# Kernel tuning notes

Measured on AMD Instinct MI355X. Metric: run time of the kernel, lower is better.

The kernel has to match this reference:

```python
import jax, jax.numpy as jnp
import numpy as np

N_LAYERS = 3
H = 128
N_NODES = 10000
N_EDGES = 160000
EPS = 1e-5

def silu(x):
    return x * jax.nn.sigmoid(x)

def batchnorm(x, gamma, beta):
    # BatchNorm1d, training-mode statistics (biased variance), over the node/edge dim
    mu = x.mean(axis=0)
    var = x.var(axis=0)
    return gamma * (x - mu) * jax.lax.rsqrt(var + EPS) + beta

def _forward(edge_index, emb_nodes, emb_edges, pre_Wn, pre_bn, pre_We, pre_be,
             We1, be1, We2, be2, Wx1, bx1, Wx2, bx2, Wh1, bh1, Wh2, bh2,
             gam_n, bet_n, gam_e, bet_e):
    src, dst = edge_index[0], edge_index[1]
    N = emb_nodes.shape[0]
    coords = emb_nodes                      # [N, 3] equivariant coordinates
    V = emb_nodes @ pre_Wn + pre_bn         # [N, H]
    E = emb_edges @ pre_We + pre_be         # [Ne, H] (overwritten by mij each layer)
    for l in range(N_LAYERS):
        diff = coords[dst] - coords[src]                          # [Ne, 3]
        dist = jnp.sqrt(jnp.sum(diff * diff, axis=-1, keepdims=True))  # [Ne, 1]
        h = jnp.concatenate([V[src], V[dst], dist, emb_edges], axis=-1)  # [Ne, 2H+3]
        mij = silu(silu(h @ We1[l] + be1[l]) @ We2[l] + be2[l])   # phi_e -> [Ne, H]
        px = silu(mij @ Wx1[l] + bx1[l]) @ Wx2[l] + bx2[l]        # phi_x -> [Ne, 3]
        # equivariant coordinate update; graph_node_index is None -> M = N
        coords = coords + jax.ops.segment_sum(diff * px, dst, num_segments=N) / (N - 1)
        mi = jax.ops.segment_sum(mij, dst, num_segments=N)        # [N, H]
        V = silu(jnp.concatenate([V, mi], axis=-1) @ Wh1[l] + bh1[l]) @ Wh2[l] + bh2[l]
        E = mij
        # encoder: act -> BatchNorm -> Dropout(eval = identity)
        V = batchnorm(jax.nn.elu(V), gam_n[l], bet_n[l])
        E = batchnorm(jax.nn.elu(E), gam_e[l], bet_e[l])
    return V, E

def setup_inputs() -> dict:
    key = jax.random.key(0)
    ks = iter(jax.random.split(key, 32))
    def rn(shape, scale=0.05):
        return jax.random.normal(next(ks), shape, dtype=jnp.float32) * scale
    src = jax.random.randint(next(ks), (N_EDGES,), 0, N_NODES)
    off = jax.random.randint(next(ks), (N_EDGES,), 1, N_NODES)
    dst = (src + off) % N_NODES  # no self-loops -> distance never exactly 0
    edge_index = jnp.stack([src, dst]).astype(jnp.int64) if jax.config.jax_enable_x64 else jnp.stack([src, dst])
    return dict(
        emb_nodes=jax.random.normal(next(ks), (N_NODES, 3), dtype=jnp.float32),
        emb_edges=jax.random.normal(next(ks), (N_EDGES, 2), dtype=jnp.float32),
        edge_index=edge_index,
        pre_Wn=rn((3, H)), pre_bn=jnp.zeros((H,), jnp.float32),
        pre_We=rn((2, H)), pre_be=jnp.zeros((H,), jnp.float32),
        We1=rn((N_LAYERS, 2 * H + 3, H)), be1=jnp.zeros((N_LAYERS, H), jnp.float32),
        We2=rn((N_LAYERS, H, H)), be2=jnp.zeros((N_LAYERS, H), jnp.float32),
        Wx1=rn((N_LAYERS, H, H)), bx1=jnp.zeros((N_LAYERS, H), jnp.float32),
        Wx2=rn((N_LAYERS, H, 3)), bx2=jnp.zeros((N_LAYERS, 3), jnp.float32),
        Wh1=rn((N_LAYERS, 2 * H, H)), bh1=jnp.zeros((N_LAYERS, H), jnp.float32),
        Wh2=rn((N_LAYERS, H, H)), bh2=jnp.zeros((N_LAYERS, H), jnp.float32),
        gam_n=jnp.ones((N_LAYERS, H), jnp.float32), bet_n=jnp.zeros((N_LAYERS, H), jnp.float32),
        gam_e=jnp.ones((N_LAYERS, H), jnp.float32), bet_e=jnp.zeros((N_LAYERS, H), jnp.float32),
    )

def reference(emb_nodes, emb_edges, edge_index, pre_Wn, pre_bn, pre_We, pre_be,
              We1, be1, We2, be2, Wx1, bx1, Wx2, bx2, Wh1, bh1, Wh2, bh2,
              gam_n, bet_n, gam_e, bet_e):
    return _forward(edge_index, emb_nodes, emb_edges, pre_Wn, pre_bn, pre_We, pre_be,
                    We1, be1, We2, be2, Wx1, bx1, Wx2, bx2, Wh1, bh1, Wh2, bh2,
                    gam_n, bet_n, gam_e, bet_e)
```

## Files before the change

kernel.cpp:

```cpp
#include <hip/hip_runtime.h>
#include <hip/hip_bf16.h>
#include <math.h>

#define NN 10000
#define NE 160000
#define HH 128
#define EPSBN 1e-5f

typedef __attribute__((ext_vector_type(8))) short s8b;
typedef __attribute__((ext_vector_type(4))) float f32x4;

#define MFMA16 __builtin_amdgcn_mfma_f32_16x16x32_bf16

__device__ __forceinline__ float silu_f(float x) { return x / (1.f + __expf(-x)); }
__device__ __forceinline__ float elu_f(float x)  { return x > 0.f ? x : expm1f(x); }

__device__ __forceinline__ ushort rnb(float x) {
    unsigned u = __float_as_uint(x);
    unsigned r = (u + 0x7fffu + ((u >> 16) & 1u)) >> 16;
    return (ushort)r;
}
__device__ __forceinline__ float bf2f(ushort u) {
    return __uint_as_float(((unsigned)u) << 16);
}
__device__ __forceinline__ s8b ldg8(const ushort* p) { return *(const s8b*)p; }

__global__ void k_zero(float* __restrict__ p, int n) {
    int i = blockIdx.x * blockDim.x + threadIdx.x;
    if (i < n) p[i] = 0.f;
}
__global__ void k_zero_int(int* __restrict__ p, int n) {
    int i = blockIdx.x * blockDim.x + threadIdx.x;
    if (i < n) p[i] = 0;
}
__global__ void k_copy(const float* __restrict__ a, float* __restrict__ b, int n) {
    int i = blockIdx.x * blockDim.x + threadIdx.x;
    if (i < n) b[i] = a[i];
}

__global__ void k_vinit(const float* __restrict__ en, const float* __restrict__ Wn,
                        const float* __restrict__ bn, ushort* __restrict__ Vb) {
    int idx = blockIdx.x * blockDim.x + threadIdx.x;
    if (idx >= NN * HH) return;
    int i = idx >> 7, j = idx & 127;
    float v = fmaf(en[i * 3 + 0], Wn[j], bn[j]);
    v = fmaf(en[i * 3 + 1], Wn[HH + j], v);
    v = fmaf(en[i * 3 + 2], Wn[2 * HH + j], v);
    Vb[idx] = rnb(v);
}

__global__ void k_wprep(const float* __restrict__ We1, const float* __restrict__ We2,
                        const float* __restrict__ Wx1, const float* __restrict__ Wh1,
                        const float* __restrict__ Wh2, ushort* __restrict__ Wb) {
    int idx = blockIdx.x * 256 + threadIdx.x;
    if (idx >= 344064) return;
    int layer = idx / 114688;
    int r = idx - layer * 114688;
    const float* src; int K; int roff;
    if (r < 32768)      { src = We1 + (size_t)layer * 33152; K = 256; roff = r; }
    else if (r < 49152) { src = We2 + (size_t)layer * 16384; K = 128; roff = r - 32768; }
    else if (r < 65536) { src = Wx1 + (size_t)layer * 16384; K = 128; roff = r - 49152; }
    else if (r < 98304) { src = Wh1 + (size_t)layer * 32768; K = 256; roff = r - 65536; }
    else                { src = Wh2 + (size_t)layer * 16384; K = 128; roff = r - 98304; }
    int n = roff / K, k = roff - n * K;
    Wb[idx] = rnb(src[k * 128 + n]);
}

__global__ void k_wx2prep(const float* __restrict__ Wx2, ushort* __restrict__ Wx2b) {
    int idx = blockIdx.x * 256 + threadIdx.x;
    if (idx >= 3 * 16 * 128) return;
    int layer = idx / 2048;
    int r = idx - layer * 2048;
    int n = r >> 7, k = r & 127;
    Wx2b[idx] = (n < 3) ? rnb(Wx2[layer * 384 + k * 3 + n]) : (ushort)0;
}

__global__ void k_hist(const int* __restrict__ dst, int* __restrict__ deg) {
    int e = blockIdx.x * blockDim.x + threadIdx.x;
    if (e < NE) atomicAdd(&deg[dst[e]], 1);
}
__global__ __launch_bounds__(256)
void k_scan(const int* __restrict__ deg, int* __restrict__ offs, int* __restrict__ cur) {
    __shared__ int part[256];
    const int t = threadIdx.x;
    const int s0 = t * 40, s1 = min(s0 + 40, NN);
    int s = 0;
    for (int i = s0; i < s1; ++i) s += deg[i];
    part[t] = s;
    __syncthreads();
    if (t == 0) {
        int r = 0;
        for (int i = 0; i < 256; ++i) { int v = part[i]; part[i] = r; r += v; }
    }
    __syncthreads();
    int r = part[t];
    for (int i = s0; i < s1; ++i) { offs[i] = r; cur[i] = r; r += deg[i]; }
    if (t == 255) offs[NN] = r;
}
__global__ void k_fill(const int* __restrict__ dst, int* __restrict__ cur, int* __restrict__ eid) {
    int e = blockIdx.x * blockDim.x + threadIdx.x;
    if (e < NE) {
        int p = atomicAdd(&cur[dst[e]], 1);
        eid[p] = e;
    }
}

__global__ __launch_bounds__(512, 2)
void k_efused(const ushort* __restrict__ Vb,
              const int* __restrict__ src, const int* __restrict__ dst,
              const float* __restrict__ coords, const float* __restrict__ ee,
              const ushort* __restrict__ W1b,
              const float* __restrict__ We1f, const float* __restrict__ be1,
              const ushort* __restrict__ W2b,
              const float* __restrict__ be2,
              const ushort* __restrict__ Wxb,
              const float* __restrict__ bx1,
              const ushort* __restrict__ Wx2b,
              const float* __restrict__ bx2,
              ushort* __restrict__ mijb, float4* __restrict__ cd4) {
    __shared__ ushort t1b[4][128][40];
    __shared__ int sid[128], did[128];
    __shared__ float dd[128], eAa[128], eBb[128];
    __shared__ float d3[3][128];
    const int t = threadIdx.x;
    const int lane = t & 63;
    const int w = t >> 6;
    const int wr = w >> 1, wc = w & 1;
    const int e0 = blockIdx.x * 128;
    if (t < 128) {
        int e = e0 + t;
        int s = src[e], d = dst[e];
        sid[t] = s; did[t] = d;
        float dx = coords[d * 3 + 0] - coords[s * 3 + 0];
        float dy = coords[d * 3 + 1] - coords[s * 3 + 1];
        float dz = coords[d * 3 + 2] - coords[s * 3 + 2];
        dd[t] = sqrtf(dx * dx + dy * dy + dz * dz);
        d3[0][t] = dx; d3[1][t] = dy; d3[2][t] = dz;
        eAa[t] = ee[2 * e]; eBb[t] = ee[2 * e + 1];
    }
    __syncthreads();
    const int l15 = lane & 15, lq = lane >> 4;
    f32x4 acc[2][4];
#pragma unroll
    for (int i = 0; i < 2; ++i)
#pragma unroll
        for (int j = 0; j < 4; ++j) acc[i][j] = (f32x4){0.f, 0.f, 0.f, 0.f};

#pragma unroll
    for (int half = 0; half < 2; ++half) {
        const int* ids = half ? did : sid;
#pragma unroll
        for (int kt = 0; kt < 4; ++kt) {
            const int wk = half * 128 + kt * 32;
            s8b a[2], b[4];
#pragma unroll
            for (int mi = 0; mi < 2; ++mi) {
                int row = ids[wr * 32 + mi * 16 + l15];
                a[mi] = ldg8(Vb + (size_t)row * HH + kt * 32 + lq * 8);
            }
#pragma unroll
            for (int ni = 0; ni < 4; ++ni) {
                int col = wc * 64 + ni * 16 + l15;
                b[ni] = ldg8(W1b + (size_t)col * 256 + wk + lq * 8);
            }
#pragma unroll
            for (int mi = 0; mi < 2; ++mi)
#pragma unroll
                for (int ni = 0; ni < 4; ++ni)
                    acc[mi][ni] = MFMA16(a[mi], b[ni], acc[mi][ni], 0, 0, 0);
        }
    }
#pragma unroll
    for (int mi = 0; mi < 2; ++mi)
#pragma unroll
        for (int ni = 0; ni < 4; ++ni) {
            int col = wc * 64 + ni * 16 + l15;
            float w256 = We1f[256 * HH + col];
            float w257 = We1f[257 * HH + col];
            float w258 = We1f[258 * HH + col];
            float bi = be1[col];
            int kt = col >> 5, c = col & 31;
#pragma unroll
            for (int r = 0; r < 4; ++r) {
                int m = wr * 32 + mi * 16 + lq * 4 + r;
                float v = acc[mi][ni][r] + bi;
                v = fmaf(dd[m], w256, v);
                v = fmaf(eAa[m], w257, v);
                v = fmaf(eBb[m], w258, v);
                t1b[kt][m][c] = rnb(silu_f(v));
                acc[mi][ni][r] = 0.f;
            }
        }
    __syncthreads();
#pragma unroll
    for (int kt = 0; kt < 4; ++kt) {
        s8b a[2], b[4];
#pragma unroll
        for (int mi = 0; mi < 2; ++mi) {
            int row = wr * 32 + mi * 16 + l15;
            a[mi] = *(const s8b*)&t1b[kt][row][lq * 8];
        }
#pragma unroll
        for (int ni = 0; ni < 4; ++ni) {
            int col = wc * 64 + ni * 16 + l15;
            b[ni] = ldg8(W2b + (size_t)col * 128 + kt * 32 + lq * 8);
        }
#pragma unroll
        for (int mi = 0; mi < 2; ++mi)
#pragma unroll
            for (int ni = 0; ni < 4; ++ni)
                acc[mi][ni] = MFMA16(a[mi], b[ni], acc[mi][ni], 0, 0, 0);
    }
    __syncthreads();
#pragma unroll
    for (int mi = 0; mi < 2; ++mi)
#pragma unroll
        for (int ni = 0; ni < 4; ++ni) {
            int col = wc * 64 + ni * 16 + l15;
            float bi = be2[col];
            int kt = col >> 5, c = col & 31;
#pragma unroll
            for (int r = 0; r < 4; ++r) {
                int m = wr * 32 + mi * 16 + lq * 4 + r;
                ushort mv = rnb(silu_f(acc[mi][ni][r] + bi));
                mijb[(size_t)(e0 + m) * HH + col] = mv;
                t1b[kt][m][c] = mv;
                acc[mi][ni][r] = 0.f;
            }
        }
    __syncthreads();
#pragma unroll
    for (int kt = 0; kt < 4; ++kt) {
        s8b a[2], b[4];
#pragma unroll
        for (int mi = 0; mi < 2; ++mi) {
            int row = wr * 32 + mi * 16 + l15;
            a[mi] = *(const s8b*)&t1b[kt][row][lq * 8];
        }
#pragma unroll
        for (int ni = 0; ni < 4; ++ni) {
            int col = wc * 64 + ni * 16 + l15;
            b[ni] = ldg8(Wxb + (size_t)col * 128 + kt * 32 + lq * 8);
        }
#pragma unroll
        for (int mi = 0; mi < 2; ++mi)
#pragma unroll
            for (int ni = 0; ni < 4; ++ni)
                acc[mi][ni] = MFMA16(a[mi], b[ni], acc[mi][ni], 0, 0, 0);
    }
    __syncthreads();
#pragma unroll
    for (int mi = 0; mi < 2; ++mi)
#pragma unroll
        for (int ni = 0; ni < 4; ++ni) {
            int col = wc * 64 + ni * 16 + l15;
            float bi = bx1[col];
            int kt = col >> 5, c = col & 31;
#pragma unroll
            for (int r = 0; r < 4; ++r) {
                int m = wr * 32 + mi * 16 + lq * 4 + r;
                t1b[kt][m][c] = rnb(silu_f(acc[mi][ni][r] + bi));
            }
        }
    __syncthreads();
    f32x4 accd = (f32x4){0.f, 0.f, 0.f, 0.f};
#pragma unroll
    for (int kt = 0; kt < 4; ++kt) {
        s8b a = *(const s8b*)&t1b[kt][w * 16 + l15][lq * 8];
        s8b b = ldg8(Wx2b + (size_t)l15 * 128 + kt * 32 + lq * 8);
        accd = MFMA16(a, b, accd, 0, 0, 0);
    }
    if (l15 < 3) {
        float bi = bx2[l15];
#pragma unroll
        for (int r = 0; r < 4; ++r) {
            int row = w * 16 + lq * 4 + r;
            float px = accd[r] + bi;
            ((float*)&cd4[e0 + row])[l15] = d3[l15][row] * px;
        }
    }
}

__global__ __launch_bounds__(128)
void k_mi(const ushort* __restrict__ mijb, const int* __restrict__ offs,
          const int* __restrict__ eid, ushort* __restrict__ mib) {
    const int n = blockIdx.x;
    const int t = threadIdx.x;
    const int b = offs[n], e = offs[n + 1];
    float s = 0.f;
    for (int j = b; j < e; ++j)
        s += bf2f(mijb[(size_t)eid[j] * HH + t]);
    mib[(size_t)n * HH + t] = rnb(s);
}

__global__ void k_coordupd(float* __restrict__ coords, const float4* __restrict__ cd4,
                           const int* __restrict__ offs, const int* __restrict__ eid) {
    int idx = blockIdx.x * blockDim.x + threadIdx.x;
    if (idx >= NN * 3) return;
    int n = idx / 3, c = idx - 3 * n;
    int b = offs[n], e = offs[n + 1];
    float s = 0.f;
    for (int j = b; j < e; ++j)
        s += ((const float*)&cd4[eid[j]])[c];
    coords[idx] += s * (1.f / (NN - 1));
}

__global__ __launch_bounds__(256, 4)
void k_nfused(const ushort* __restrict__ Vb, const ushort* __restrict__ mib,
              const ushort* __restrict__ Whb,
              const float* __restrict__ bh1,
              const ushort* __restrict__ Wgb,
              const float* __restrict__ bh2,
              float* __restrict__ X,
              float* __restrict__ ssum, float* __restrict__ ssq) {
    __shared__ ushort tb[4][64][40];
    const int t = threadIdx.x;
    const int lane = t & 63;
    const int w = t >> 6;
    const int wr = w >> 1, wc = w & 1;
    const int r0 = blockIdx.x * 64;
    const int l15 = lane & 15, lq = lane >> 4;
    f32x4 acc[2][4];
#pragma unroll
    for (int i = 0; i < 2; ++i)
#pragma unroll
        for (int j = 0; j < 4; ++j) acc[i][j] = (f32x4){0.f, 0.f, 0.f, 0.f};

#pragma unroll
    for (int kk = 0; kk < 8; ++kk) {
        const ushort* Ap = (kk < 4) ? Vb : mib;
        const int k0 = (kk & 3) * 32;
        s8b a[2], b[4];
#pragma unroll
        for (int mi_ = 0; mi_ < 2; ++mi_) {
            int row = r0 + wr * 32 + mi_ * 16 + l15;
            if (row >= NN) row = NN - 1;
            a[mi_] = ldg8(Ap + (size_t)row * HH + k0 + lq * 8);
        }
#pragma unroll
        for (int ni = 0; ni < 4; ++ni) {
            int col = wc * 64 + ni * 16 + l15;
            b[ni] = ldg8(Whb + (size_t)col * 256 + kk * 32 + lq * 8);
        }
#pragma unroll
        for (int mi_ = 0; mi_ < 2; ++mi_)
#pragma unroll
            for (int ni = 0; ni < 4; ++ni)
                acc[mi_][ni] = MFMA16(a[mi_], b[ni], acc[mi_][ni], 0, 0, 0);
    }
#pragma unroll
    for (int mi_ = 0; mi_ < 2; ++mi_)
#pragma unroll
        for (int ni = 0; ni < 4; ++ni) {
            int col = wc * 64 + ni * 16 + l15;
            float bi = bh1[col];
            int kt = col >> 5, c = col & 31;
#pragma unroll
            for (int r = 0; r < 4; ++r) {
                int m = wr * 32 + mi_ * 16 + lq * 4 + r;
                tb[kt][m][c] = rnb(silu_f(acc[mi_][ni][r] + bi));
                acc[mi_][ni][r] = 0.f;
            }
        }
    __syncthreads();
#pragma unroll
    for (int kt = 0; kt < 4; ++kt) {
        s8b a[2], b[4];
#pragma unroll
        for (int mi_ = 0; mi_ < 2; ++mi_) {
            int row = wr * 32 + mi_ * 16 + l15;
            a[mi_] = *(const s8b*)&tb[kt][row][lq * 8];
        }
#pragma unroll
        for (int ni = 0; ni < 4; ++ni) {
            int col = wc * 64 + ni * 16 + l15;
            b[ni] = ldg8(Wgb + (size_t)col * 128 + kt * 32 + lq * 8);
        }
#pragma unroll
        for (int mi_ = 0; mi_ < 2; ++mi_)
#pragma unroll
            for (int ni = 0; ni < 4; ++ni)
                acc[mi_][ni] = MFMA16(a[mi_], b[ni], acc[mi_][ni], 0, 0, 0);
    }
    float s[4] = {0.f, 0.f, 0.f, 0.f}, q[4] = {0.f, 0.f, 0.f, 0.f};
#pragma unroll
    for (int mi_ = 0; mi_ < 2; ++mi_)
#pragma unroll
        for (int ni = 0; ni < 4; ++ni) {
            int col = wc * 64 + ni * 16 + l15;
            float bi = bh2[col];
#pragma unroll
            for (int r = 0; r < 4; ++r) {
                int m = r0 + wr * 32 + mi_ * 16 + lq * 4 + r;
                float v = elu_f(acc[mi_][ni][r] + bi);
                if (m < NN) {
                    X[(size_t)m * HH + col] = v;
                    s[ni] += v; q[ni] += v * v;
                }
            }
        }
#pragma unroll
    for (int j = 0; j < 4; ++j) {
        s[j] += __shfl_xor(s[j], 16);
        s[j] += __shfl_xor(s[j], 32);
        q[j] += __shfl_xor(q[j], 16);
        q[j] += __shfl_xor(q[j], 32);
    }
    if (lane < 16) {
#pragma unroll
        for (int j = 0; j < 4; ++j) {
            int col = wc * 64 + j * 16 + l15;
            atomicAdd(&ssum[col], s[j]);
            atomicAdd(&ssq[col], q[j]);
        }
    }
}

__global__ void k_bnorm_nodes(const float* __restrict__ X, const float* __restrict__ ssum,
                              const float* __restrict__ ssq, const float* __restrict__ gam,
                              const float* __restrict__ bet, float* __restrict__ outf,
                              ushort* __restrict__ outb, int writeb) {
    int idx = blockIdx.x * blockDim.x + threadIdx.x;
    if (idx >= NN * HH) return;
    int c = idx & 127;
    float mu = ssum[c] * (1.f / NN);
    float var = ssq[c] * (1.f / NN) - mu * mu;
    float v = fmaf(gam[c] * (X[idx] - mu), rsqrtf(var + EPSBN), bet[c]);
    if (writeb) outb[idx] = rnb(v);
    else        outf[idx] = v;
}

__global__ __launch_bounds__(256)
void k_estats(const ushort* __restrict__ mijb, float* __restrict__ ssum, float* __restrict__ ssq) {
    const int t = threadIdx.x;
    const int col = t & 127;
    const int half = t >> 7;
    const int rbase = blockIdx.x * 250;
    float s = 0.f, q = 0.f;
    for (int r = rbase + half; r < rbase + 250; r += 2) {
        float x = elu_f(bf2f(mijb[(size_t)r * HH + col]));
        s += x; q += x * x;
    }
    atomicAdd(&ssum[col], s);
    atomicAdd(&ssq[col], q);
}

__global__ void k_bnorm_edges(const ushort* __restrict__ mijb, const float* __restrict__ ssum,
                              const float* __restrict__ ssq, const float* __restrict__ gam,
                              const float* __restrict__ bet, float* __restrict__ out) {
    size_t stride = (size_t)gridDim.x * blockDim.x;
    for (size_t idx = (size_t)blockIdx.x * blockDim.x + threadIdx.x; idx < (size_t)NE * HH; idx += stride) {
        int c = (int)(idx & 127);
        float x = elu_f(bf2f(mijb[idx]));
        float mu = ssum[c] * (1.f / NE);
        float var = ssq[c] * (1.f / NE) - mu * mu;
        out[idx] = fmaf(gam[c] * (x - mu), rsqrtf(var + EPSBN), bet[c]);
    }
}

extern "C" void kernel_launch(void* const* d_in, const int* in_sizes, int n_in,
                              void* d_out, int out_size, void* d_ws, size_t ws_size,
                              hipStream_t stream) {
    (void)in_sizes; (void)n_in; (void)out_size; (void)ws_size;
    const float* emb_nodes = (const float*)d_in[0];
    const float* emb_edges = (const float*)d_in[1];
    const int*   eidx      = (const int*)d_in[2];
    const float* pre_Wn = (const float*)d_in[3];
    const float* pre_bn = (const float*)d_in[4];
    const float* We1 = (const float*)d_in[7];
    const float* be1 = (const float*)d_in[8];
    const float* We2 = (const float*)d_in[9];
    const float* be2 = (const float*)d_in[10];
    const float* Wx1 = (const float*)d_in[11];
    const float* bx1 = (const float*)d_in[12];
    const float* Wx2 = (const float*)d_in[13];
    const float* bx2 = (const float*)d_in[14];
    const float* Wh1 = (const float*)d_in[15];
    const float* bh1 = (const float*)d_in[16];
    const float* Wh2 = (const float*)d_in[17];
    const float* bh2 = (const float*)d_in[18];
    const float* gam_n = (const float*)d_in[19];
    const float* bet_n = (const float*)d_in[20];
    const float* gam_e = (const float*)d_in[21];
    const float* bet_e = (const float*)d_in[22];

    const int* src = eidx;
    const int* dst = eidx + NE;

    float* ws = (float*)d_ws;
    float*   coords = ws;
    ushort*  Vb     = (ushort*)(ws + 30000);
    ushort*  mib    = (ushort*)(ws + 670000);
    float*   X      = ws + 1310000;
    float4*  cd4    = (float4*)(ws + 2590000);
    ushort*  mijb   = (ushort*)(ws + 3230000);
    float*   snN    = ws + 13470000;
    float*   sqN    = ws + 13470128;
    float*   snE    = ws + 13470256;
    float*   sqE    = ws + 13470384;
    ushort*  Wb     = (ushort*)(ws + 13470512);
    ushort*  Wx2b   = (ushort*)(ws + 13642544);
    int*     I0     = (int*)(ws + 13645616);
    int*     deg    = I0;
    int*     offs   = I0 + 10000;
    int*     cur    = I0 + 20001;
    int*     eid    = I0 + 30001;

    float* outV = (float*)d_out;
    float* outE = (float*)d_out + (size_t)NN * HH;

    k_copy<<<(30000 + 255) / 256, 256, 0, stream>>>(emb_nodes, coords, 30000);
    k_vinit<<<(NN * HH + 255) / 256, 256, 0, stream>>>(emb_nodes, pre_Wn, pre_bn, Vb);
    k_wprep<<<1344, 256, 0, stream>>>(We1, We2, Wx1, Wh1, Wh2, Wb);
    k_wx2prep<<<24, 256, 0, stream>>>(Wx2, Wx2b);

    k_zero_int<<<(NN + 255) / 256, 256, 0, stream>>>(deg, NN);
    k_hist<<<(NE + 255) / 256, 256, 0, stream>>>(dst, deg);
    k_scan<<<1, 256, 0, stream>>>(deg, offs, cur);
    k_fill<<<(NE + 255) / 256, 256, 0, stream>>>(dst, cur, eid);

    for (int l = 0; l < 3; ++l) {
        const float* We1l = We1 + (size_t)l * 259 * 128;
        const float* be1l = be1 + l * 128;
        const float* be2l = be2 + l * 128;
        const float* bx1l = bx1 + l * 128;
        const float* bx2l = bx2 + l * 3;
        const float* bh1l = bh1 + l * 128;
        const float* bh2l = bh2 + l * 128;
        const size_t L = (size_t)l * 114688;
        const ushort* W1b = Wb + L;
        const ushort* W2b = Wb + L + 32768;
        const ushort* Wxb = Wb + L + 49152;
        const ushort* Whb = Wb + L + 65536;
        const ushort* Wgb = Wb + L + 98304;
        const ushort* Wx2bl = Wx2b + (size_t)l * 2048;

        k_zero<<<2, 256, 0, stream>>>(snN, 512);
        k_efused<<<NE / 128, 512, 0, stream>>>(Vb, src, dst, coords, emb_edges,
                                               W1b, We1l, be1l, W2b, be2l,
                                               Wxb, bx1l, Wx2bl, bx2l, mijb, cd4);
        k_mi<<<NN, 128, 0, stream>>>(mijb, offs, eid, mib);
        k_coordupd<<<(NN * 3 + 255) / 256, 256, 0, stream>>>(coords, cd4, offs, eid);
        k_nfused<<<(NN + 63) / 64, 256, 0, stream>>>(Vb, mib, Whb, bh1l, Wgb, bh2l, X, snN, sqN);
        k_bnorm_nodes<<<(NN * HH + 255) / 256, 256, 0, stream>>>(X, snN, sqN, gam_n + l * 128,
                                                                 bet_n + l * 128,
                                                                 outV, Vb, (l < 2) ? 1 : 0);
        if (l == 2) {
            k_estats<<<640, 256, 0, stream>>>(mijb, snE, sqE);
            k_bnorm_edges<<<4096, 256, 0, stream>>>(mijb, snE, sqE, gam_e + l * 128, bet_e + l * 128, outE);
        }
    }
}
```

Baseline: 843.6 us.

## Software-pipeline MFMA operand loads and shrink node-MLP tile to 32 rows

In the edge MLP kernel, the gathered V rows and weight fragments are now double-buffered in registers, so the next k-step's global loads are in flight while the current MFMAs run. The src/dst indices go straight into registers instead of through shared memory, and the per-column We1 tail weights are hoisted ahead of the first barrier. The node MLP kernel switches to 32-row tiles with one M fragment per wave, launching twice as many blocks to raise parallelism. BN stat zeroing becomes a single launch over per-layer buffers, and bf16 rounding uses the library conversion, at the cost of extra registers for the prefetch buffers.

```diff
diff --git a/kernel.cpp b/kernel.cpp
--- a/kernel.cpp
+++ b/kernel.cpp
@@ -15,15 +15,14 @@
 __device__ __forceinline__ float silu_f(float x) { return x / (1.f + __expf(-x)); }
 __device__ __forceinline__ float elu_f(float x)  { return x > 0.f ? x : expm1f(x); }
 
-__device__ __forceinline__ ushort rnb(float x) {
-    unsigned u = __float_as_uint(x);
-    unsigned r = (u + 0x7fffu + ((u >> 16) & 1u)) >> 16;
-    return (ushort)r;
+__device__ __forceinline__ ushort f2b(float x) {
+    __hip_bfloat16 h = __float2bfloat16(x);
+    return *reinterpret_cast<ushort*>(&h);
 }
 __device__ __forceinline__ float bf2f(ushort u) {
     return __uint_as_float(((unsigned)u) << 16);
 }
-__device__ __forceinline__ s8b ldg8(const ushort* p) { return *(const s8b*)p; }
+__device__ __forceinline__ s8b ldg8(const ushort* p) { return *(const s8b*)(p); }
 
 __global__ void k_zero(float* __restrict__ p, int n) {
     int i = blockIdx.x * blockDim.x + threadIdx.x;
@@ -46,7 +45,7 @@
     float v = fmaf(en[i * 3 + 0], Wn[j], bn[j]);
     v = fmaf(en[i * 3 + 1], Wn[HH + j], v);
     v = fmaf(en[i * 3 + 2], Wn[2 * HH + j], v);
-    Vb[idx] = rnb(v);
+    Vb[idx] = f2b(v);
 }
 
 __global__ void k_wprep(const float* __restrict__ We1, const float* __restrict__ We2,
@@ -63,7 +62,7 @@
     else if (r < 98304) { src = Wh1 + (size_t)layer * 32768; K = 256; roff = r - 65536; }
     else                { src = Wh2 + (size_t)layer * 16384; K = 128; roff = r - 98304; }
     int n = roff / K, k = roff - n * K;
-    Wb[idx] = rnb(src[k * 128 + n]);
+    Wb[idx] = f2b(src[k * 128 + n]);
 }
 
 __global__ void k_wx2prep(const float* __restrict__ Wx2, ushort* __restrict__ Wx2b) {
@@ -72,7 +71,7 @@
     int layer = idx / 2048;
     int r = idx - layer * 2048;
     int n = r >> 7, k = r & 127;
-    Wx2b[idx] = (n < 3) ? rnb(Wx2[layer * 384 + k * 3 + n]) : (ushort)0;
+    Wx2b[idx] = (n < 3) ? f2b(Wx2[layer * 384 + k * 3 + n]) : (ushort)0;
 }
 
 __global__ void k_hist(const int* __restrict__ dst, int* __restrict__ deg) {
@@ -119,7 +118,6 @@
               const float* __restrict__ bx2,
               ushort* __restrict__ mijb, float4* __restrict__ cd4) {
     __shared__ ushort t1b[4][128][40];
-    __shared__ int sid[128], did[128];
     __shared__ float dd[128], eAa[128], eBb[128];
     __shared__ float d3[3][128];
     const int t = threadIdx.x;
@@ -127,10 +125,26 @@
     const int w = t >> 6;
     const int wr = w >> 1, wc = w & 1;
     const int e0 = blockIdx.x * 128;
+    const int l15 = lane & 15, lq = lane >> 4;
+
+    const int er0 = e0 + wr * 32 + l15;
+    const int er1 = er0 + 16;
+    const int rS0 = src[er0], rS1 = src[er1];
+    const int rD0 = dst[er0], rD1 = dst[er1];
+
+    float w256[4], w257[4], w258[4], bi1[4];
+#pragma unroll
+    for (int ni = 0; ni < 4; ++ni) {
+        int col = wc * 64 + ni * 16 + l15;
+        w256[ni] = We1f[256 * HH + col];
+        w257[ni] = We1f[257 * HH + col];
+        w258[ni] = We1f[258 * HH + col];
+        bi1[ni]  = be1[col];
+    }
+
     if (t < 128) {
         int e = e0 + t;
         int s = src[e], d = dst[e];
-        sid[t] = s; did[t] = d;
         float dx = coords[d * 3 + 0] - coords[s * 3 + 0];
         float dy = coords[d * 3 + 1] - coords[s * 3 + 1];
         float dz = coords[d * 3 + 2] - coords[s * 3 + 2];
@@ -138,78 +152,89 @@
         d3[0][t] = dx; d3[1][t] = dy; d3[2][t] = dz;
         eAa[t] = ee[2 * e]; eBb[t] = ee[2 * e + 1];
     }
-    __syncthreads();
-    const int l15 = lane & 15, lq = lane >> 4;
+
     f32x4 acc[2][4];
 #pragma unroll
     for (int i = 0; i < 2; ++i)
 #pragma unroll
         for (int j = 0; j < 4; ++j) acc[i][j] = (f32x4){0.f, 0.f, 0.f, 0.f};
 
-#pragma unroll
-    for (int half = 0; half < 2; ++half) {
-        const int* ids = half ? did : sid;
-#pragma unroll
-        for (int kt = 0; kt < 4; ++kt) {
-            const int wk = half * 128 + kt * 32;
-            s8b a[2], b[4];
-#pragma unroll
-            for (int mi = 0; mi < 2; ++mi) {
-                int row = ids[wr * 32 + mi * 16 + l15];
-                a[mi] = ldg8(Vb + (size_t)row * HH + kt * 32 + lq * 8);
-            }
-#pragma unroll
-            for (int ni = 0; ni < 4; ++ni) {
-                int col = wc * 64 + ni * 16 + l15;
-                b[ni] = ldg8(W1b + (size_t)col * 256 + wk + lq * 8);
-            }
-#pragma unroll
-            for (int mi = 0; mi < 2; ++mi)
-#pragma unroll
-                for (int ni = 0; ni < 4; ++ni)
-                    acc[mi][ni] = MFMA16(a[mi], b[ni], acc[mi][ni], 0, 0, 0);
-        }
-    }
+    const ushort* wb1 = W1b + (size_t)(wc * 64 + l15) * 256 + lq * 8;
+    s8b a0 = ldg8(Vb + (size_t)rS0 * HH + lq * 8);
+    s8b a1 = ldg8(Vb + (size_t)rS1 * HH + lq * 8);
+    s8b b0 = ldg8(wb1);
+    s8b b1 = ldg8(wb1 + 16 * 256);
+    s8b b2 = ldg8(wb1 + 32 * 256);
+    s8b b3 = ldg8(wb1 + 48 * 256);
+#pragma unroll
+    for (int s = 0; s < 8; ++s) {
+        s8b na0, na1, nb0, nb1, nb2, nb3;
+        if (s < 7) {
+            const int sn = s + 1;
+            const int kt = sn & 3;
+            const int r0 = (sn < 4) ? rS0 : rD0;
+            const int r1 = (sn < 4) ? rS1 : rD1;
+            na0 = ldg8(Vb + (size_t)r0 * HH + kt * 32 + lq * 8);
+            na1 = ldg8(Vb + (size_t)r1 * HH + kt * 32 + lq * 8);
+            nb0 = ldg8(wb1 + sn * 32);
+            nb1 = ldg8(wb1 + 16 * 256 + sn * 32);
+            nb2 = ldg8(wb1 + 32 * 256 + sn * 32);
+            nb3 = ldg8(wb1 + 48 * 256 + sn * 32);
+        }
+        acc[0][0] = MFMA16(a0, b0, acc[0][0], 0, 0, 0);
+        acc[0][1] = MFMA16(a0, b1, acc[0][1], 0, 0, 0);
+        acc[0][2] = MFMA16(a0, b2, acc[0][2], 0, 0, 0);
+        acc[0][3] = MFMA16(a0, b3, acc[0][3], 0, 0, 0);
+        acc[1][0] = MFMA16(a1, b0, acc[1][0], 0, 0, 0);
+        acc[1][1] = MFMA16(a1, b1, acc[1][1], 0, 0, 0);
+        acc[1][2] = MFMA16(a1, b2, acc[1][2], 0, 0, 0);
+        acc[1][3] = MFMA16(a1, b3, acc[1][3], 0, 0, 0);
+        if (s < 7) { a0 = na0; a1 = na1; b0 = nb0; b1 = nb1; b2 = nb2; b3 = nb3; }
+    }
+    __syncthreads();
 #pragma unroll
     for (int mi = 0; mi < 2; ++mi)
 #pragma unroll
         for (int ni = 0; ni < 4; ++ni) {
             int col = wc * 64 + ni * 16 + l15;
-            float w256 = We1f[256 * HH + col];
-            float w257 = We1f[257 * HH + col];
-            float w258 = We1f[258 * HH + col];
-            float bi = be1[col];
             int kt = col >> 5, c = col & 31;
 #pragma unroll
             for (int r = 0; r < 4; ++r) {
                 int m = wr * 32 + mi * 16 + lq * 4 + r;
-                float v = acc[mi][ni][r] + bi;
-                v = fmaf(dd[m], w256, v);
-                v = fmaf(eAa[m], w257, v);
-                v = fmaf(eBb[m], w258, v);
-                t1b[kt][m][c] = rnb(silu_f(v));
+                float v = acc[mi][ni][r] + bi1[ni];
+                v = fmaf(dd[m], w256[ni], v);
+                v = fmaf(eAa[m], w257[ni], v);
+                v = fmaf(eBb[m], w258[ni], v);
+                t1b[kt][m][c] = f2b(silu_f(v));
                 acc[mi][ni][r] = 0.f;
             }
         }
+    const ushort* wb2 = W2b + (size_t)(wc * 64 + l15) * 128 + lq * 8;
+    b0 = ldg8(wb2);
+    b1 = ldg8(wb2 + 16 * 128);
+    b2 = ldg8(wb2 + 32 * 128);
+    b3 = ldg8(wb2 + 48 * 128);
     __syncthreads();
 #pragma unroll
     for (int kt = 0; kt < 4; ++kt) {
-        s8b a[2], b[4];
-#pragma unroll
-        for (int mi = 0; mi < 2; ++mi) {
-            int row = wr * 32 + mi * 16 + l15;
-            a[mi] = *(const s8b*)&t1b[kt][row][lq * 8];
-        }
-#pragma unroll
-        for (int ni = 0; ni < 4; ++ni) {
-            int col = wc * 64 + ni * 16 + l15;
-            b[ni] = ldg8(W2b + (size_t)col * 128 + kt * 32 + lq * 8);
-        }
-#pragma unroll
-        for (int mi = 0; mi < 2; ++mi)
-#pragma unroll
-            for (int ni = 0; ni < 4; ++ni)
-                acc[mi][ni] = MFMA16(a[mi], b[ni], acc[mi][ni], 0, 0, 0);
+        s8b a0c = *(const s8b*)&t1b[kt][wr * 32 + l15][lq * 8];
+        s8b a1c = *(const s8b*)&t1b[kt][wr * 32 + 16 + l15][lq * 8];
+        s8b nb0, nb1, nb2, nb3;
+        if (kt < 3) {
+            nb0 = ldg8(wb2 + (kt + 1) * 32);
+            nb1 = ldg8(wb2 + 16 * 128 + (kt + 1) * 32);
+            nb2 = ldg8(wb2 + 32 * 128 + (kt + 1) * 32);
+            nb3 = ldg8(wb2 + 48 * 128 + (kt + 1) * 32);
+        }
+        acc[0][0] = MFMA16(a0c, b0, acc[0][0], 0, 0, 0);
+        acc[0][1] = MFMA16(a0c, b1, acc[0][1], 0, 0, 0);
+        acc[0][2] = MFMA16(a0c, b2, acc[0][2], 0, 0, 0);
+        acc[0][3] = MFMA16(a0c, b3, acc[0][3], 0, 0, 0);
+        acc[1][0] = MFMA16(a1c, b0, acc[1][0], 0, 0, 0);
+        acc[1][1] = MFMA16(a1c, b1, acc[1][1], 0, 0, 0);
+        acc[1][2] = MFMA16(a1c, b2, acc[1][2], 0, 0, 0);
+        acc[1][3] = MFMA16(a1c, b3, acc[1][3], 0, 0, 0);
+        if (kt < 3) { b0 = nb0; b1 = nb1; b2 = nb2; b3 = nb3; }
     }
     __syncthreads();
 #pragma unroll
@@ -222,31 +247,38 @@
 #pragma unroll
             for (int r = 0; r < 4; ++r) {
                 int m = wr * 32 + mi * 16 + lq * 4 + r;
-                ushort mv = rnb(silu_f(acc[mi][ni][r] + bi));
+                ushort mv = f2b(silu_f(acc[mi][ni][r] + bi));
                 mijb[(size_t)(e0 + m) * HH + col] = mv;
                 t1b[kt][m][c] = mv;
                 acc[mi][ni][r] = 0.f;
             }
         }
+    const ushort* wbx = Wxb + (size_t)(wc * 64 + l15) * 128 + lq * 8;
+    b0 = ldg8(wbx);
+    b1 = ldg8(wbx + 16 * 128);
+    b2 = ldg8(wbx + 32 * 128);
+    b3 = ldg8(wbx + 48 * 128);
     __syncthreads();
 #pragma unroll
     for (int kt = 0; kt < 4; ++kt) {
-        s8b a[2], b[4];
-#pragma unroll
-        for (int mi = 0; mi < 2; ++mi) {
-            int row = wr * 32 + mi * 16 + l15;
-            a[mi] = *(const s8b*)&t1b[kt][row][lq * 8];
-        }
-#pragma unroll
-        for (int ni = 0; ni < 4; ++ni) {
-            int col = wc * 64 + ni * 16 + l15;
-            b[ni] = ldg8(Wxb + (size_t)col * 128 + kt * 32 + lq * 8);
-        }
-#pragma unroll
-        for (int mi = 0; mi < 2; ++mi)
-#pragma unroll
-            for (int ni = 0; ni < 4; ++ni)
-                acc[mi][ni] = MFMA16(a[mi], b[ni], acc[mi][ni], 0, 0, 0);
+        s8b a0c = *(const s8b*)&t1b[kt][wr * 32 + l15][lq * 8];
+        s8b a1c = *(const s8b*)&t1b[kt][wr * 32 + 16 + l15][lq * 8];
+        s8b nb0, nb1, nb2, nb3;
+        if (kt < 3) {
+            nb0 = ldg8(wbx + (kt + 1) * 32);
+            nb1 = ldg8(wbx + 16 * 128 + (kt + 1) * 32);
+            nb2 = ldg8(wbx + 32 * 128 + (kt + 1) * 32);
+            nb3 = ldg8(wbx + 48 * 128 + (kt + 1) * 32);
+        }
+        acc[0][0] = MFMA16(a0c, b0, acc[0][0], 0, 0, 0);
+        acc[0][1] = MFMA16(a0c, b1, acc[0][1], 0, 0, 0);
+        acc[0][2] = MFMA16(a0c, b2, acc[0][2], 0, 0, 0);
+        acc[0][3] = MFMA16(a0c, b3, acc[0][3], 0, 0, 0);
+        acc[1][0] = MFMA16(a1c, b0, acc[1][0], 0, 0, 0);
+        acc[1][1] = MFMA16(a1c, b1, acc[1][1], 0, 0, 0);
+        acc[1][2] = MFMA16(a1c, b2, acc[1][2], 0, 0, 0);
+        acc[1][3] = MFMA16(a1c, b3, acc[1][3], 0, 0, 0);
+        if (kt < 3) { b0 = nb0; b1 = nb1; b2 = nb2; b3 = nb3; }
     }
     __syncthreads();
 #pragma unroll
@@ -259,7 +291,7 @@
 #pragma unroll
             for (int r = 0; r < 4; ++r) {
                 int m = wr * 32 + mi * 16 + lq * 4 + r;
-                t1b[kt][m][c] = rnb(silu_f(acc[mi][ni][r] + bi));
+                t1b[kt][m][c] = f2b(silu_f(acc[mi][ni][r] + bi));
             }
         }
     __syncthreads();
@@ -290,7 +322,7 @@
     float s = 0.f;
     for (int j = b; j < e; ++j)
         s += bf2f(mijb[(size_t)eid[j] * HH + t]);
-    mib[(size_t)n * HH + t] = rnb(s);
+    mib[(size_t)n * HH + t] = f2b(s);
 }
 
 __global__ void k_coordupd(float* __restrict__ coords, const float4* __restrict__ cd4,
@@ -313,92 +345,93 @@
               const float* __restrict__ bh2,
               float* __restrict__ X,
               float* __restrict__ ssum, float* __restrict__ ssq) {
-    __shared__ ushort tb[4][64][40];
+    __shared__ ushort tb[4][32][40];
     const int t = threadIdx.x;
     const int lane = t & 63;
     const int w = t >> 6;
     const int wr = w >> 1, wc = w & 1;
-    const int r0 = blockIdx.x * 64;
+    const int r0 = blockIdx.x * 32;
     const int l15 = lane & 15, lq = lane >> 4;
-    f32x4 acc[2][4];
-#pragma unroll
-    for (int i = 0; i < 2; ++i)
-#pragma unroll
-        for (int j = 0; j < 4; ++j) acc[i][j] = (f32x4){0.f, 0.f, 0.f, 0.f};
-
-#pragma unroll
-    for (int kk = 0; kk < 8; ++kk) {
-        const ushort* Ap = (kk < 4) ? Vb : mib;
-        const int k0 = (kk & 3) * 32;
-        s8b a[2], b[4];
-#pragma unroll
-        for (int mi_ = 0; mi_ < 2; ++mi_) {
-            int row = r0 + wr * 32 + mi_ * 16 + l15;
-            if (row >= NN) row = NN - 1;
-            a[mi_] = ldg8(Ap + (size_t)row * HH + k0 + lq * 8);
-        }
-#pragma unroll
-        for (int ni = 0; ni < 4; ++ni) {
-            int col = wc * 64 + ni * 16 + l15;
-            b[ni] = ldg8(Whb + (size_t)col * 256 + kk * 32 + lq * 8);
-        }
-#pragma unroll
-        for (int mi_ = 0; mi_ < 2; ++mi_)
-#pragma unroll
-            for (int ni = 0; ni < 4; ++ni)
-                acc[mi_][ni] = MFMA16(a[mi_], b[ni], acc[mi_][ni], 0, 0, 0);
-    }
-#pragma unroll
-    for (int mi_ = 0; mi_ < 2; ++mi_)
-#pragma unroll
-        for (int ni = 0; ni < 4; ++ni) {
-            int col = wc * 64 + ni * 16 + l15;
-            float bi = bh1[col];
-            int kt = col >> 5, c = col & 31;
-#pragma unroll
-            for (int r = 0; r < 4; ++r) {
-                int m = wr * 32 + mi_ * 16 + lq * 4 + r;
-                tb[kt][m][c] = rnb(silu_f(acc[mi_][ni][r] + bi));
-                acc[mi_][ni][r] = 0.f;
+    int rowA = r0 + wr * 16 + l15;
+    if (rowA >= NN) rowA = NN - 1;
+    f32x4 acc[4];
+#pragma unroll
+    for (int j = 0; j < 4; ++j) acc[j] = (f32x4){0.f, 0.f, 0.f, 0.f};
+
+    const ushort* wbh = Whb + (size_t)(wc * 64 + l15) * 256 + lq * 8;
+    s8b a0 = ldg8(Vb + (size_t)rowA * HH + lq * 8);
+    s8b b0 = ldg8(wbh);
+    s8b b1 = ldg8(wbh + 16 * 256);
+    s8b b2 = ldg8(wbh + 32 * 256);
+    s8b b3 = ldg8(wbh + 48 * 256);
+#pragma unroll
+    for (int s = 0; s < 8; ++s) {
+        s8b na0, nb0, nb1, nb2, nb3;
+        if (s < 7) {
+            const int sn = s + 1;
+            const ushort* Ap = (sn < 4) ? Vb : mib;
+            const int k0 = (sn & 3) * 32;
+            na0 = ldg8(Ap + (size_t)rowA * HH + k0 + lq * 8);
+            nb0 = ldg8(wbh + sn * 32);
+            nb1 = ldg8(wbh + 16 * 256 + sn * 32);
+            nb2 = ldg8(wbh + 32 * 256 + sn * 32);
+            nb3 = ldg8(wbh + 48 * 256 + sn * 32);
+        }
+        acc[0] = MFMA16(a0, b0, acc[0], 0, 0, 0);
+        acc[1] = MFMA16(a0, b1, acc[1], 0, 0, 0);
+        acc[2] = MFMA16(a0, b2, acc[2], 0, 0, 0);
+        acc[3] = MFMA16(a0, b3, acc[3], 0, 0, 0);
+        if (s < 7) { a0 = na0; b0 = nb0; b1 = nb1; b2 = nb2; b3 = nb3; }
+    }
+#pragma unroll
+    for (int ni = 0; ni < 4; ++ni) {
+        int col = wc * 64 + ni * 16 + l15;
+        float bi = bh1[col];
+        int kt = col >> 5, c = col & 31;
+#pragma unroll
+        for (int r = 0; r < 4; ++r) {
+            int m = wr * 16 + lq * 4 + r;
+            tb[kt][m][c] = f2b(silu_f(acc[ni][r] + bi));
+            acc[ni][r] = 0.f;
+        }
+    }
+    const ushort* wbg = Wgb + (size_t)(wc * 64 + l15) * 128 + lq * 8;
+    b0 = ldg8(wbg);
+    b1 = ldg8(wbg + 16 * 128);
+    b2 = ldg8(wbg + 32 * 128);
+    b3 = ldg8(wbg + 48 * 128);
+    __syncthreads();
+#pragma unroll
+    for (int kt = 0; kt < 4; ++kt) {
+        s8b a = *(const s8b*)&tb[kt][wr * 16 + l15][lq * 8];
+        s8b nb0, nb1, nb2, nb3;
+        if (kt < 3) {
+            nb0 = ldg8(wbg + (kt + 1) * 32);
+            nb1 = ldg8(wbg + 16 * 128 + (kt + 1) * 32);
+            nb2 = ldg8(wbg + 32 * 128 + (kt + 1) * 32);
+            nb3 = ldg8(wbg + 48 * 128 + (kt + 1) * 32);
+        }
+        acc[0] = MFMA16(a, b0, acc[0], 0, 0, 0);
+        acc[1] = MFMA16(a, b1, acc[1], 0, 0, 0);
+        acc[2] = MFMA16(a, b2, acc[2], 0, 0, 0);
+        acc[3] = MFMA16(a, b3, acc[3], 0, 0, 0);
+        if (kt < 3) { b0 = nb0; b1 = nb1; b2 = nb2; b3 = nb3; }
+    }
+    float s[4] = {0.f, 0.f, 0.f, 0.f}, q[4] = {0.f, 0.f, 0.f, 0.f};
+#pragma unroll
+    for (int ni = 0; ni < 4; ++ni) {
+        int col = wc * 64 + ni * 16 + l15;
+        float bi = bh2[col];
+#pragma unroll
+        for (int r = 0; r < 4; ++r) {
+            int m = r0 + wr * 16 + lq * 4 + r;
+            float v = elu_f(acc[ni][r] + bi);
+            if (m < NN) {
+                X[(size_t)m * HH + col] = v;
+                s[ni] += v; q[ni] += v * v;
             }
         }
-    __syncthreads();
-#pragma unroll
-    for (int kt = 0; kt < 4; ++kt) {
-        s8b a[2], b[4];
-#pragma unroll
-        for (int mi_ = 0; mi_ < 2; ++mi_) {
-            int row = wr * 32 + mi_ * 16 + l15;
-            a[mi_] = *(const s8b*)&tb[kt][row][lq * 8];
-        }
-#pragma unroll
-        for (int ni = 0; ni < 4; ++ni) {
-            int col = wc * 64 + ni * 16 + l15;
-            b[ni] = ldg8(Wgb + (size_t)col * 128 + kt * 32 + lq * 8);
-        }
-#pragma unroll
-        for (int mi_ = 0; mi_ < 2; ++mi_)
-#pragma unroll
-            for (int ni = 0; ni < 4; ++ni)
-                acc[mi_][ni] = MFMA16(a[mi_], b[ni], acc[mi_][ni], 0, 0, 0);
-    }
-    float s[4] = {0.f, 0.f, 0.f, 0.f}, q[4] = {0.f, 0.f, 0.f, 0.f};
-#pragma unroll
-    for (int mi_ = 0; mi_ < 2; ++mi_)
-#pragma unroll
-        for (int ni = 0; ni < 4; ++ni) {
-            int col = wc * 64 + ni * 16 + l15;
-            float bi = bh2[col];
-#pragma unroll
-            for (int r = 0; r < 4; ++r) {
-                int m = r0 + wr * 32 + mi_ * 16 + lq * 4 + r;
-                float v = elu_f(acc[mi_][ni][r] + bi);
-                if (m < NN) {
-                    X[(size_t)m * HH + col] = v;
-                    s[ni] += v; q[ni] += v * v;
-                }
-            }
-        }
+    }
 #pragma unroll
     for (int j = 0; j < 4; ++j) {
         s[j] += __shfl_xor(s[j], 16);
@@ -426,7 +459,7 @@
     float mu = ssum[c] * (1.f / NN);
     float var = ssq[c] * (1.f / NN) - mu * mu;
     float v = fmaf(gam[c] * (X[idx] - mu), rsqrtf(var + EPSBN), bet[c]);
-    if (writeb) outb[idx] = rnb(v);
+    if (writeb) outb[idx] = f2b(v);
     else        outf[idx] = v;
 }
 
@@ -494,13 +527,11 @@
     float*   X      = ws + 1310000;
     float4*  cd4    = (float4*)(ws + 2590000);
     ushort*  mijb   = (ushort*)(ws + 3230000);
-    float*   snN    = ws + 13470000;
-    float*   sqN    = ws + 13470128;
-    float*   snE    = ws + 13470256;
-    float*   sqE    = ws + 13470384;
-    ushort*  Wb     = (ushort*)(ws + 13470512);
-    ushort*  Wx2b   = (ushort*)(ws + 13642544);
-    int*     I0     = (int*)(ws + 13645616);
+    float*   statN  = ws + 13470000;
+    float*   statE  = ws + 13470768;
+    ushort*  Wb     = (ushort*)(ws + 13471024);
+    ushort*  Wx2b   = (ushort*)(ws + 13643056);
+    int*     I0     = (int*)(ws + 13646128);
     int*     deg    = I0;
     int*     offs   = I0 + 10000;
     int*     cur    = I0 + 20001;
@@ -513,6 +544,7 @@
     k_vinit<<<(NN * HH + 255) / 256, 256, 0, stream>>>(emb_nodes, pre_Wn, pre_bn, Vb);
     k_wprep<<<1344, 256, 0, stream>>>(We1, We2, Wx1, Wh1, Wh2, Wb);
     k_wx2prep<<<24, 256, 0, stream>>>(Wx2, Wx2b);
+    k_zero<<<4, 256, 0, stream>>>(statN, 1024);
 
     k_zero_int<<<(NN + 255) / 256, 256, 0, stream>>>(deg, NN);
     k_hist<<<(NE + 255) / 256, 256, 0, stream>>>(dst, deg);
@@ -534,20 +566,22 @@
         const ushort* Whb = Wb + L + 65536;
         const ushort* Wgb = Wb + L + 98304;
         const ushort* Wx2bl = Wx2b + (size_t)l * 2048;
-
-        k_zero<<<2, 256, 0, stream>>>(snN, 512);
+        float* snN = statN + (size_t)l * 256;
+        float* sqN = snN + 128;
+
         k_efused<<<NE / 128, 512, 0, stream>>>(Vb, src, dst, coords, emb_edges,
                                                W1b, We1l, be1l, W2b, be2l,
                                                Wxb, bx1l, Wx2bl, bx2l, mijb, cd4);
         k_mi<<<NN, 128, 0, stream>>>(mijb, offs, eid, mib);
         k_coordupd<<<(NN * 3 + 255) / 256, 256, 0, stream>>>(coords, cd4, offs, eid);
-        k_nfused<<<(NN + 63) / 64, 256, 0, stream>>>(Vb, mib, Whb, bh1l, Wgb, bh2l, X, snN, sqN);
+        k_nfused<<<(NN + 31) / 32, 256, 0, stream>>>(Vb, mib, Whb, bh1l, Wgb, bh2l, X, snN, sqN);
         k_bnorm_nodes<<<(NN * HH + 255) / 256, 256, 0, stream>>>(X, snN, sqN, gam_n + l * 128,
                                                                  bet_n + l * 128,
                                                                  outV, Vb, (l < 2) ? 1 : 0);
         if (l == 2) {
-            k_estats<<<640, 256, 0, stream>>>(mijb, snE, sqE);
-            k_bnorm_edges<<<4096, 256, 0, stream>>>(mijb, snE, sqE, gam_e + l * 128, bet_e + l * 128, outE);
-        }
-    }
-}
+            k_estats<<<640, 256, 0, stream>>>(mijb, statE, statE + 128);
+            k_bnorm_edges<<<4096, 256, 0, stream>>>(mijb, statE, statE + 128,
+                                                    gam_e + l * 128, bet_e + l * 128, outE);
+        }
+    }
+}
```

After: 837.1 us. About the same (-0.8%).
